# Performance work log

Measured on AMD Instinct MI355X. Metric: run time of the kernel, lower is better.

The kernel has to match this reference:

```python
import jax, jax.numpy as jnp
import numpy as np

V_TH = 1.0
LENS, SCALE, HIGHT, GAMMA = 0.5, 6.0, 0.15, 0.5  # MultiGaussian surrogate constants (DH-SNN)


def _gauss(x, mu, sigma):
    return jnp.exp(-((x - mu) ** 2) / (2.0 * sigma ** 2)) / (jnp.sqrt(2.0 * jnp.pi) * sigma)


@jax.custom_vjp
def spike_fn(x):
    return (x > 0).astype(x.dtype)


def _spike_fwd(x):
    return spike_fn(x), x


def _spike_bwd(x, g):
    sg = GAMMA * (_gauss(x, 0.0, LENS) * (1.0 + HIGHT)
                  - _gauss(x, LENS, SCALE * LENS) * HIGHT
                  - _gauss(x, -LENS, SCALE * LENS) * HIGHT)
    return (g * sg,)


spike_fn.defvjp(_spike_fwd, _spike_bwd)


def setup_inputs() -> dict:
    key = jax.random.key(0)
    ks = jax.random.split(key, 12)
    B, T, I, H, O = 128, 784, 512, 512, 10
    xavier_in = lambda k, sh: jax.random.normal(k, sh, jnp.float32) * jnp.sqrt(2.0 / (sh[0] + sh[1]))
    return {
        'input_data': jax.random.normal(ks[0], (B, T, I), jnp.float32),
        'W1': xavier_in(ks[1], (H, I)),
        'b1': jnp.zeros((H,), jnp.float32),
        'W2': xavier_in(ks[2], (H, I)),
        'b2': jnp.zeros((H,), jnp.float32),
        'tau_m': jax.random.uniform(ks[3], (H,), jnp.float32, 0.0, 4.0),
        'tau_n1': jax.random.uniform(ks[4], (H,), jnp.float32, 2.0, 6.0),
        'tau_n2': jax.random.uniform(ks[5], (H,), jnp.float32, -4.0, 0.0),
        'Wr': xavier_in(ks[6], (O, H)),
        'br': jnp.zeros((O,), jnp.float32),
        'mem0': jax.random.uniform(ks[7], (B, H), jnp.float32),
        'spike0': jax.random.uniform(ks[8], (B, H), jnp.float32),
    }


def reference(input_data, W1, b1, W2, b2, tau_m, tau_n1, tau_n2, Wr, br, mem0, spike0):
    # Batched branch projections for all timesteps (big GEMMs, done once)
    d1_all = jnp.einsum('bti,hi->bth', input_data, W1) + b1  # [B,T,H]
    d2_all = jnp.einsum('bti,hi->bth', input_data, W2) + b2

    alpha = jax.nn.sigmoid(tau_m)    # membrane decay
    beta1 = jax.nn.sigmoid(tau_n1)   # branch-1 dendritic decay
    beta2 = jax.nn.sigmoid(tau_n2)   # branch-2 dendritic decay

    B, H = mem0.shape
    d1_init = jnp.zeros((B, H), input_data.dtype)
    d2_init = jnp.zeros((B, H), input_data.dtype)

    def step(carry, xs):
        mem, spk, d1, d2 = carry
        d1_t, d2_t = xs
        d1 = beta1 * d1 + (1.0 - beta1) * d1_t
        d2 = beta2 * d2 + (1.0 - beta2) * d2_t
        total = d1 + d2
        mem = mem * alpha + (1.0 - alpha) * total - V_TH * spk
        spk = spike_fn(mem - V_TH)
        return (mem, spk, d1, d2), spk

    xs = (jnp.swapaxes(d1_all, 0, 1), jnp.swapaxes(d2_all, 0, 1))  # [T,B,H]
    _, spikes = jax.lax.scan(step, (mem0, spike0, d1_init, d2_init), xs)
    spikes = jnp.swapaxes(spikes, 0, 1)  # [B,T,H]
    out = jnp.einsum('bth,oh->bto', spikes, Wr) + br  # readout per timestep
    return out
```

## Files before the change

kernel.cpp:

```cpp
#include <hip/hip_runtime.h>
#include <cmath>

#define HD 512
#define IN 512
#define TT 784
#define BB 128
#define MH 50176

typedef short short8 __attribute__((ext_vector_type(8)));
typedef unsigned short ushort8 __attribute__((ext_vector_type(8)));
typedef float floatx4 __attribute__((ext_vector_type(4)));
typedef unsigned int uintx4 __attribute__((ext_vector_type(4)));

#define GLDS(gp, lp) __builtin_amdgcn_global_load_lds( \
    (const __attribute__((address_space(1))) void*)(gp), \
    (__attribute__((address_space(3))) void*)(lp), 16, 0, 0)

#define CVTPK(d, a, b) asm("v_cvt_pk_bf16_f32 %0, %1, %2" : "=v"(d) : "v"(a), "v"(b))

__device__ __forceinline__ unsigned short bf16_rne(float x) {
    unsigned u = __float_as_uint(x);
    unsigned r = u + 0x7FFFu + ((u >> 16) & 1u);
    return (unsigned short)(r >> 16);
}
__device__ __forceinline__ float bf16_f(unsigned short s) {
    return __uint_as_float(((unsigned)s) << 16);
}

__global__ __launch_bounds__(256) void split3(
    const float* __restrict__ src, unsigned short* __restrict__ p1,
    unsigned short* __restrict__ p2, unsigned short* __restrict__ p3, long n8)
{
    long g = (long)blockIdx.x * 256 + threadIdx.x;
    if (g >= n8) return;
    const float* xp = src + g * 8;
    ushort8 o1, o2, o3;
#pragma unroll
    for (int j = 0; j < 8; ++j) {
        float x = xp[j];
        unsigned short s1 = bf16_rne(x);
        float r1 = x - bf16_f(s1);
        unsigned short s2 = bf16_rne(r1);
        float r2 = r1 - bf16_f(s2);
        unsigned short s3 = bf16_rne(r2);
        o1[j] = s1; o2[j] = s2; o3[j] = s3;
    }
    *(ushort8*)(p1 + g * 8) = o1;
    *(ushort8*)(p2 + g * 8) = o2;
    *(ushort8*)(p3 + g * 8) = o3;
}

__global__ __launch_bounds__(256, 2) void gemm_fused(
    const float* __restrict__ Xf,
    const unsigned short* __restrict__ Wp,
    const float* __restrict__ b1, const float* __restrict__ b2,
    float* __restrict__ d1buf, float* __restrict__ d2buf)
{
    __shared__ unsigned short lds[6][128][32];
    unsigned short* lflat = &lds[0][0][0];
    const int tid  = threadIdx.x;
    const int lane = tid & 63;
    const int w    = tid >> 6;
    const int wg = (blockIdx.x & 7) * 392 + (blockIdx.x >> 3);
    const int pm = wg >> 3;
    const int pn = wg & 7;
    const int m0 = pm * 128;
    const int n0 = pn * 128;

    const unsigned short* gpb[6];
    unsigned lofb[6];
    {
        const int rsub = lane >> 2;
        const int csub = (lane & 3) * 8;
#pragma unroll
        for (int j = 0; j < 6; ++j) {
            int s = w * 6 + j;
            int p = s >> 3, sub = s & 7;
            gpb[j] = Wp + ((size_t)p * 1024 + n0 + sub * 16 + rsub) * IN + csub;
            lofb[j] = 12288u + (unsigned)s * 512;
        }
    }

    const int arow  = tid >> 1;
    const int ahalf = tid & 1;
    const float* ga = Xf + (size_t)(m0 + arow) * IN + ahalf * 16;
    const int awbase = arow * 32 + ahalf * 16;

    floatx4 acc[4][4];
#pragma unroll
    for (int i = 0; i < 4; ++i)
#pragma unroll
        for (int j = 0; j < 4; ++j) acc[i][j] = (floatx4){0.f, 0.f, 0.f, 0.f};

    const int wm = w >> 1, wn = w & 1;
    const int c16 = lane & 15;
    const int q8  = (lane >> 4) * 8;

#define LOADA(DST, T) do {                                           \
    _Pragma("unroll")                                                \
    for (int q = 0; q < 4; ++q)                                      \
        DST[q] = *(const floatx4*)(ga + (T) * 32 + q * 4);           \
    } while (0)

#define SPLITW(SRC) do {                                             \
    unsigned w1[8], w2[8], w3[8];                                    \
    _Pragma("unroll")                                                \
    for (int q = 0; q < 4; ++q) {                                    \
        _Pragma("unroll")                                            \
        for (int e = 0; e < 2; ++e) {                                \
            float x0 = SRC[q][e * 2], x1 = SRC[q][e * 2 + 1];        \
            unsigned pk1, pk2, pk3;                                  \
            CVTPK(pk1, x0, x1);                                      \
            float r0 = x0 - __uint_as_float(pk1 << 16);              \
            float r1 = x1 - __uint_as_float(pk1 & 0xFFFF0000u);      \
            CVTPK(pk2, r0, r1);                                      \
            float s0 = r0 - __uint_as_float(pk2 << 16);              \
            float s1 = r1 - __uint_as_float(pk2 & 0xFFFF0000u);      \
            CVTPK(pk3, s0, s1);                                      \
            w1[q * 2 + e] = pk1; w2[q * 2 + e] = pk2; w3[q * 2 + e] = pk3; \
        }                                                            \
    }                                                                \
    *(uintx4*)(lflat + awbase)            = (uintx4){w1[0], w1[1], w1[2], w1[3]}; \
    *(uintx4*)(lflat + awbase + 8)        = (uintx4){w1[4], w1[5], w1[6], w1[7]}; \
    *(uintx4*)(lflat + 4096 + awbase)     = (uintx4){w2[0], w2[1], w2[2], w2[3]}; \
    *(uintx4*)(lflat + 4096 + awbase + 8) = (uintx4){w2[4], w2[5], w2[6], w2[7]}; \
    *(uintx4*)(lflat + 8192 + awbase)     = (uintx4){w3[0], w3[1], w3[2], w3[3]}; \
    *(uintx4*)(lflat + 8192 + awbase + 8) = (uintx4){w3[4], w3[5], w3[6], w3[7]}; \
    } while (0)

#define COMPUTE() do {                                               \
    short8 Bf[3][4];                                                 \
    _Pragma("unroll")                                                \
    for (int p = 0; p < 3; ++p)                                      \
        _Pragma("unroll")                                            \
        for (int fj = 0; fj < 4; ++fj)                               \
            Bf[p][fj] = *(const short8*)&lds[3 + p][wn * 64 + fj * 16 + c16][q8]; \
    _Pragma("unroll")                                                \
    for (int fi = 0; fi < 4; ++fi) {                                 \
        const int r = wm * 64 + fi * 16 + c16;                       \
        short8 a1 = *(const short8*)&lds[0][r][q8];                  \
        short8 a2 = *(const short8*)&lds[1][r][q8];                  \
        short8 a3 = *(const short8*)&lds[2][r][q8];                  \
        _Pragma("unroll")                                            \
        for (int fj = 0; fj < 4; ++fj) {                             \
            floatx4 c = acc[fi][fj];                                 \
            c = __builtin_amdgcn_mfma_f32_16x16x32_bf16(a3, Bf[0][fj], c, 0, 0, 0); \
            c = __builtin_amdgcn_mfma_f32_16x16x32_bf16(a2, Bf[1][fj], c, 0, 0, 0); \
            c = __builtin_amdgcn_mfma_f32_16x16x32_bf16(a1, Bf[2][fj], c, 0, 0, 0); \
            c = __builtin_amdgcn_mfma_f32_16x16x32_bf16(a2, Bf[0][fj], c, 0, 0, 0); \
            c = __builtin_amdgcn_mfma_f32_16x16x32_bf16(a1, Bf[1][fj], c, 0, 0, 0); \
            c = __builtin_amdgcn_mfma_f32_16x16x32_bf16(a1, Bf[0][fj], c, 0, 0, 0); \
            acc[fi][fj] = c;                                         \
        }                                                            \
    } } while (0)

#define BAR() asm volatile("s_barrier" ::: "memory")

    floatx4 xa[4], xb[4];
    LOADA(xa, 0);

#pragma unroll 1
    for (int tp = 0; tp < 8; ++tp) {
        const int t0 = tp * 2, t1 = tp * 2 + 1;
#pragma unroll
        for (int j = 0; j < 6; ++j) GLDS(gpb[j] + t0 * 32, lflat + lofb[j]);
        LOADA(xb, t1);
        SPLITW(xa);
        asm volatile("s_waitcnt vmcnt(4) lgkmcnt(0)" ::: "memory");
        BAR();
        COMPUTE();
        BAR();
#pragma unroll
        for (int j = 0; j < 6; ++j) GLDS(gpb[j] + t1 * 32, lflat + lofb[j]);
        if (tp < 7) LOADA(xa, t1 + 1);
        SPLITW(xb);
        if (tp < 7) asm volatile("s_waitcnt vmcnt(4) lgkmcnt(0)" ::: "memory");
        else        asm volatile("s_waitcnt vmcnt(0) lgkmcnt(0)" ::: "memory");
        BAR();
        COMPUTE();
        BAR();
    }
#undef LOADA
#undef SPLITW
#undef COMPUTE
#undef BAR

    const int quad = lane >> 4;
    const bool first = (n0 < HD);
    const float* bias = first ? b1 : b2;
    float* obuf = first ? d1buf : d2buf;
    const int nb = n0 & (HD - 1);
    float bv[4];
#pragma unroll
    for (int fj = 0; fj < 4; ++fj) bv[fj] = bias[nb + wn * 64 + fj * 16 + c16];
#pragma unroll
    for (int fi = 0; fi < 4; ++fi) {
#pragma unroll
        for (int fj = 0; fj < 4; ++fj) {
            int n = nb + wn * 64 + fj * 16 + c16;
#pragma unroll
            for (int r = 0; r < 4; ++r) {
                int m = m0 + wm * 64 + fi * 16 + quad * 4 + r;
                obuf[(size_t)m * HD + n] = acc[fi][fj][r] + bv[fj];
            }
        }
    }
}

#define LOADG(g, A1, A2) do {                                        \
    _Pragma("unroll")                                                \
    for (int i = 0; i < 16; ++i) {                                   \
        A1[i] = p1[(size_t)((g) * 16 + i) * HD];                     \
        A2[i] = p2[(size_t)((g) * 16 + i) * HD];                     \
    } } while (0)

#define COMPG(g, A1, A2) do {                                        \
    unsigned int wq = 0;                                             \
    _Pragma("unroll")                                                \
    for (int i = 0; i < 16; ++i) {                                   \
        d1 = be1 * d1 + (1.f - be1) * A1[i];                         \
        d2 = be2 * d2 + (1.f - be2) * A2[i];                         \
        float tot = d1 + d2;                                         \
        mem = mem * alpha + (1.f - alpha) * tot - spk;               \
        bool fire = (mem - 1.0f) > 0.f;                              \
        spk = fire ? 1.f : 0.f;                                      \
        wq |= (fire ? 1u : 0u) << i;                                 \
    }                                                                \
    sp[(size_t)(g) * HD] = (unsigned short)wq; } while (0)

__global__ __launch_bounds__(64) void scan_half(
    const float* __restrict__ d1buf, const float* __restrict__ d2buf,
    const float* __restrict__ tau_m, const float* __restrict__ tau_n1,
    const float* __restrict__ tau_n2,
    const float* __restrict__ mem0, const float* __restrict__ spike0,
    unsigned short* __restrict__ spikes, int b0)
{
    const int gid = blockIdx.x * 64 + threadIdx.x;
    const int h  = gid & (HD - 1);
    const int bl = gid >> 9;
    const int b  = b0 + bl;
    const float alpha = 1.f / (1.f + expf(-tau_m[h]));
    const float be1   = 1.f / (1.f + expf(-tau_n1[h]));
    const float be2   = 1.f / (1.f + expf(-tau_n2[h]));
    float mem = mem0[b * HD + h];
    float spk = spike0[b * HD + h];
    float d1 = 0.f, d2 = 0.f;
    const float* p1 = d1buf + (size_t)bl * TT * HD + h;
    const float* p2 = d2buf + (size_t)bl * TT * HD + h;
    unsigned short* sp = spikes + (size_t)b * (TT / 16) * HD + h;

    float a1A[16], a2A[16], a1B[16], a2B[16];
    LOADG(0, a1A, a2A);
#pragma unroll 1
    for (int g = 0; g < 48; g += 2) {
        LOADG(g + 1, a1B, a2B);
        COMPG(g,     a1A, a2A);
        LOADG(g + 2, a1A, a2A);
        COMPG(g + 1, a1B, a2B);
    }
    COMPG(48, a1A, a2A);
}

__global__ __launch_bounds__(256) void readout(
    const unsigned short* __restrict__ spikes,
    const float* __restrict__ Wr, const float* __restrict__ br,
    float* __restrict__ out)
{
    __shared__ float WrS[10 * HD];
    __shared__ float brS[10];
    const int tid = threadIdx.x;
    for (int i = tid; i < 10 * HD; i += 256) WrS[i] = Wr[i];
    if (tid < 10) brS[tid] = br[tid];
    __syncthreads();

    const int gid = blockIdx.x * 256 + tid;
    const int t = gid % TT;
    const int b = gid / TT;
    const int tw  = t >> 4;
    const int bit = t & 15;
    const unsigned short* row = spikes + ((size_t)b * (TT / 16) + tw) * HD;

    float acc[10];
#pragma unroll
    for (int o = 0; o < 10; ++o) acc[o] = brS[o];

    for (int h = 0; h < HD; ++h) {
        float s = (float)((row[h] >> bit) & 1);
#pragma unroll
        for (int o = 0; o < 10; ++o) acc[o] = fmaf(s, WrS[o * HD + h], acc[o]);
    }
    float* op = out + (size_t)gid * 10;
#pragma unroll
    for (int o = 0; o < 10; ++o) op[o] = acc[o];
}

extern "C" void kernel_launch(void* const* d_in, const int* in_sizes, int n_in,
                              void* d_out, int out_size, void* d_ws, size_t ws_size,
                              hipStream_t stream)
{
    const float* X      = (const float*)d_in[0];
    const float* W1     = (const float*)d_in[1];
    const float* b1     = (const float*)d_in[2];
    const float* W2     = (const float*)d_in[3];
    const float* b2     = (const float*)d_in[4];
    const float* tau_m  = (const float*)d_in[5];
    const float* tau_n1 = (const float*)d_in[6];
    const float* tau_n2 = (const float*)d_in[7];
    const float* Wr     = (const float*)d_in[8];
    const float* br     = (const float*)d_in[9];
    const float* mem0   = (const float*)d_in[10];
    const float* spike0 = (const float*)d_in[11];
    float* out = (float*)d_out;

    char* p = (char*)d_ws;
    unsigned short* Wp = (unsigned short*)p;  p += (size_t)3 * 1024 * IN * 2;
    float* d1buf = (float*)p;                 p += (size_t)MH * HD * 4;
    float* d2buf = (float*)p;                 p += (size_t)MH * HD * 4;
    unsigned short* spikes = (unsigned short*)p;

    const size_t WPS = (size_t)1024 * IN;

    split3<<<dim3(128), dim3(256), 0, stream>>>(
        W1, Wp, Wp + WPS, Wp + 2 * WPS, (long)HD * IN / 8);
    split3<<<dim3(128), dim3(256), 0, stream>>>(
        W2, Wp + (size_t)HD * IN, Wp + WPS + (size_t)HD * IN,
        Wp + 2 * WPS + (size_t)HD * IN, (long)HD * IN / 8);

    for (int half = 0; half < 2; ++half) {
        gemm_fused<<<dim3(392 * 8), dim3(256), 0, stream>>>(
            X + (size_t)half * MH * IN, Wp, b1, b2, d1buf, d2buf);
        scan_half<<<dim3(512), dim3(64), 0, stream>>>(
            d1buf, d2buf, tau_m, tau_n1, tau_n2, mem0, spike0,
            spikes, half * 64);
    }
    readout<<<dim3(BB * TT / 256), dim3(256), 0, stream>>>(spikes, Wr, br, out);
}
```

Before: 937.8 us.

## Run GEMM and scan over full batch when workspace allows; vectorize readout loads

When the workspace is large enough, the GEMM and scan run once over all 128 batch rows instead of in two halves. The scan then launches 1024 single-wave blocks rather than 512, which doubles the parallelism of the latency-bound serial scan. The readout kernel now loads spike words as 8-wide vectors. The full path needs twice the intermediate buffer memory and falls back to the halved path when the workspace is too small.

```diff
diff --git a/kernel.cpp b/kernel.cpp
--- a/kernel.cpp
+++ b/kernel.cpp
@@ -6,6 +6,7 @@
 #define TT 784
 #define BB 128
 #define MH 50176
+#define MF 100352
 
 typedef short short8 __attribute__((ext_vector_type(8)));
 typedef unsigned short ushort8 __attribute__((ext_vector_type(8)));
@@ -54,14 +55,14 @@
     const float* __restrict__ Xf,
     const unsigned short* __restrict__ Wp,
     const float* __restrict__ b1, const float* __restrict__ b2,
-    float* __restrict__ d1buf, float* __restrict__ d2buf)
+    float* __restrict__ d1buf, float* __restrict__ d2buf, int nmt)
 {
     __shared__ unsigned short lds[6][128][32];
     unsigned short* lflat = &lds[0][0][0];
     const int tid  = threadIdx.x;
     const int lane = tid & 63;
     const int w    = tid >> 6;
-    const int wg = (blockIdx.x & 7) * 392 + (blockIdx.x >> 3);
+    const int wg = (blockIdx.x & 7) * nmt + (blockIdx.x >> 3);
     const int pm = wg >> 3;
     const int pn = wg & 7;
     const int m0 = pm * 128;
@@ -228,7 +229,7 @@
     }                                                                \
     sp[(size_t)(g) * HD] = (unsigned short)wq; } while (0)
 
-__global__ __launch_bounds__(64) void scan_half(
+__global__ __launch_bounds__(64) void scan_k(
     const float* __restrict__ d1buf, const float* __restrict__ d2buf,
     const float* __restrict__ tau_m, const float* __restrict__ tau_n1,
     const float* __restrict__ tau_n2,
@@ -278,16 +279,23 @@
     const int b = gid / TT;
     const int tw  = t >> 4;
     const int bit = t & 15;
-    const unsigned short* row = spikes + ((size_t)b * (TT / 16) + tw) * HD;
+    const ushort8* row8 = (const ushort8*)(spikes +
+        ((size_t)b * (TT / 16) + tw) * HD);
 
     float acc[10];
 #pragma unroll
     for (int o = 0; o < 10; ++o) acc[o] = brS[o];
 
-    for (int h = 0; h < HD; ++h) {
-        float s = (float)((row[h] >> bit) & 1);
-#pragma unroll
-        for (int o = 0; o < 10; ++o) acc[o] = fmaf(s, WrS[o * HD + h], acc[o]);
+#pragma unroll 1
+    for (int hh = 0; hh < HD / 8; ++hh) {
+        ushort8 v = row8[hh];
+#pragma unroll
+        for (int j = 0; j < 8; ++j) {
+            float s = (float)((v[j] >> bit) & 1);
+            const int h = hh * 8 + j;
+#pragma unroll
+            for (int o = 0; o < 10; ++o) acc[o] = fmaf(s, WrS[o * HD + h], acc[o]);
+        }
     }
     float* op = out + (size_t)gid * 10;
 #pragma unroll
@@ -312,13 +320,19 @@
     const float* spike0 = (const float*)d_in[11];
     float* out = (float*)d_out;
 
+    const size_t WPB   = (size_t)3 * 1024 * IN * 2;
+    const size_t DFULL = (size_t)MF * HD * 4;
+    const size_t DHALF = (size_t)MH * HD * 4;
+    const size_t SPB   = (size_t)BB * (TT / 16) * HD * 2;
+    const size_t WPS   = (size_t)1024 * IN;
+
+    const bool full = ws_size >= WPB + 2 * DFULL + SPB;
+
     char* p = (char*)d_ws;
-    unsigned short* Wp = (unsigned short*)p;  p += (size_t)3 * 1024 * IN * 2;
-    float* d1buf = (float*)p;                 p += (size_t)MH * HD * 4;
-    float* d2buf = (float*)p;                 p += (size_t)MH * HD * 4;
+    unsigned short* Wp = (unsigned short*)p;  p += WPB;
+    float* d1buf = (float*)p;                 p += full ? DFULL : DHALF;
+    float* d2buf = (float*)p;                 p += full ? DFULL : DHALF;
     unsigned short* spikes = (unsigned short*)p;
-
-    const size_t WPS = (size_t)1024 * IN;
 
     split3<<<dim3(128), dim3(256), 0, stream>>>(
         W1, Wp, Wp + WPS, Wp + 2 * WPS, (long)HD * IN / 8);
@@ -326,12 +340,19 @@
         W2, Wp + (size_t)HD * IN, Wp + WPS + (size_t)HD * IN,
         Wp + 2 * WPS + (size_t)HD * IN, (long)HD * IN / 8);
 
-    for (int half = 0; half < 2; ++half) {
-        gemm_fused<<<dim3(392 * 8), dim3(256), 0, stream>>>(
-            X + (size_t)half * MH * IN, Wp, b1, b2, d1buf, d2buf);
-        scan_half<<<dim3(512), dim3(64), 0, stream>>>(
-            d1buf, d2buf, tau_m, tau_n1, tau_n2, mem0, spike0,
-            spikes, half * 64);
+    if (full) {
+        gemm_fused<<<dim3(784 * 8), dim3(256), 0, stream>>>(
+            X, Wp, b1, b2, d1buf, d2buf, 784);
+        scan_k<<<dim3(1024), dim3(64), 0, stream>>>(
+            d1buf, d2buf, tau_m, tau_n1, tau_n2, mem0, spike0, spikes, 0);
+    } else {
+        for (int half = 0; half < 2; ++half) {
+            gemm_fused<<<dim3(392 * 8), dim3(256), 0, stream>>>(
+                X + (size_t)half * MH * IN, Wp, b1, b2, d1buf, d2buf, 392);
+            scan_k<<<dim3(512), dim3(64), 0, stream>>>(
+                d1buf, d2buf, tau_m, tau_n1, tau_n2, mem0, spike0,
+                spikes, half * 64);
+        }
     }
     readout<<<dim3(BB * TT / 256), dim3(256), 0, stream>>>(spikes, Wr, br, out);
 }
```

Result: faster. 912.5 us (-2.7%).
